# Kernel tuning notes

Measured on AMD Instinct MI355X. Metric: run time of the kernel, lower is better.

The kernel has to match this reference:

```python
import jax, jax.numpy as jnp
import numpy as np
from jax import lax

KS = 10      # kernel_size (asserted == 10 in the torch module)
DCT_N = 10   # dct_n


def _dct_pair(N):
    k = np.arange(N)[:, None]
    i = np.arange(N)[None, :]
    w = np.full((N, 1), np.sqrt(2.0 / N))
    w[0, 0] = np.sqrt(1.0 / N)
    d = w * np.cos(np.pi * (i + 0.5) * k / N)
    return jnp.asarray(d, jnp.float32), jnp.asarray(np.linalg.inv(d), jnp.float32)


def _conv1d(x, w):
    # x: [B, C, L], w: [O, C, K], VALID conv (bias=False in torch)
    return lax.conv_general_dilated(x, w, (1,), 'VALID',
                                    dimension_numbers=('NCH', 'OIH', 'NCH'))


def _two_conv(x, w1, w2):
    return jax.nn.relu(_conv1d(jax.nn.relu(_conv1d(x, w1)), w2))


def _gconv(x, w, att, b):
    # GraphConvolution: att @ (x @ w) + b ; x: [B, node, f_in]
    return jnp.einsum('nm,bmo->bno', att, jnp.einsum('bmf,fo->bmo', x, w)) + b


def _gcn(x, gc1_w, gc1_att, gc1_b, gcb_w, gcb_att, gcb_b, gc7_w, gc7_att, gc7_b):
    # Standard motion-prediction GCN (eval mode: BN=identity, dropout off)
    y = jnp.tanh(_gconv(x, gc1_w, gc1_att, gc1_b))
    for s in range(gcb_w.shape[0]):  # small fixed num_stage
        h = jnp.tanh(_gconv(y, gcb_w[s, 0], gcb_att[s, 0], gcb_b[s, 0]))
        h = jnp.tanh(_gconv(h, gcb_w[s, 1], gcb_att[s, 1], gcb_b[s, 1]))
        y = y + h
    return _gconv(y, gc7_w, gc7_att, gc7_b) + x


def _ffc(x, wl, wg):
    # RealFFC(dim=3): spectral branch (rFFT over time, 1x1 conv on real/imag,
    # ReLU, irFFT) + local 1x1 branch. x: [B, 3, F/3, T]
    y = jnp.fft.rfft(x, axis=-1)
    yc = jnp.concatenate([y.real, y.imag], axis=1)            # [B, 6, F/3, K]
    yc = jax.nn.relu(jnp.einsum('oc,bcfk->bofk', wg, yc))
    re, im = jnp.split(yc, 2, axis=1)
    spec = jnp.fft.irfft(re + 1j * im, n=x.shape[-1], axis=-1)
    return jnp.einsum('oc,bcft->boft', wl, x) + spec


def _forward(input_seq, wq1, wq2, wk1, wk2,
             gc1_w, gc1_att, gc1_b, gcb_w, gcb_att, gcb_b,
             gc7_w, gc7_att, gc7_b, mlp_w1, mlp_w2, ffc_wl, ffc_wg,
             output_n, input_n):
    seq = input_seq[:, :input_n]
    B, _, F = seq.shape
    blen = KS + output_n                       # DCT block length (30)
    dctm, idctm = _dct_pair(blen)
    key_seq = jnp.swapaxes(seq, 1, 2)[:, :, :input_n - output_n]
    query_seq = jnp.swapaxes(seq, 1, 2)[:, :, -KS:]
    # im2col-style overlapping temporal blocks -> per-block DCT
    nvb = input_n - blen + 1
    idx = np.arange(blen)[None, :] + np.arange(nvb)[:, None]
    blocks = seq[:, idx]                       # [B, nvb, blen, F]
    # matches torch reshape(...,dct_n,-1).transpose(2,3).reshape: feature-major
    dvb = jnp.einsum('dk,bnkf->bnfd', dctm[:DCT_N], blocks).reshape(B, nvb, -1)
    key_feat = _two_conv(key_seq / 1000.0, wk1, wk2)       # [B, D, nvb]
    query_feat = _two_conv(query_seq / 1000.0, wq1, wq2)   # [B, D, 1]
    score = jnp.einsum('bdq,bdk->bqk', query_feat, key_feat) + 1e-15
    attn = score / jnp.sum(score, axis=2, keepdims=True)   # sum-normalized attention
    attended = jnp.einsum('bqk,bkf->bqf', attn, dvb)[:, 0].reshape(B, F, DCT_N)
    # FFC branch: pad with last frame x10, fold F into (3, F//3)
    ffc_in = jnp.concatenate([seq, jnp.repeat(seq[:, -1:], 10, axis=1)], axis=1)
    ffc_in = jnp.swapaxes(ffc_in, 1, 2).reshape(B, 3, F // 3, input_n + 10)
    ffc_out = _ffc(ffc_in, ffc_wl, ffc_wg).reshape(B, F, input_n + 10)[:, :, :DCT_N]
    ffc_out = jnp.swapaxes(ffc_out, 1, 2)      # [B, DCT_N, F]
    # GCN branch: last KS frames + last frame repeated output_n times
    gidx = np.concatenate([np.arange(input_n - KS, input_n),
                           np.full(output_n, input_n - 1)])
    gcn_in = seq[:, gidx]                      # [B, blen, F]
    dct_in = jnp.einsum('dk,bkf->bfd', dctm[:DCT_N], gcn_in)
    gcn_out = _gcn(dct_in, gc1_w, gc1_att, gc1_b, gcb_w, gcb_att, gcb_b,
                   gc7_w, gc7_att, gc7_b)      # [B, F, DCT_N]
    combined = jnp.concatenate([gcn_out, attended], axis=-1)
    recon = jnp.einsum('kd,bfd->bkf', idctm[:, :DCT_N], combined[:, :, :DCT_N])  # [B, blen, F]
    fused = jnp.swapaxes(jnp.concatenate([recon, ffc_out], axis=1), 1, 2)  # [B, F, blen+DCT_N=40]
    h = jax.nn.relu(jnp.einsum('bft,ot->bfo', fused, mlp_w1))  # Linear(40,256), no bias
    out = jnp.einsum('bfo,to->bft', h, mlp_w2)                 # Linear(256,40), no bias
    out = jnp.swapaxes(out, 1, 2)[:, :DCT_N]   # [B, DCT_N, F]
    return out[:, :, None, :]                  # [B, DCT_N, itera=1, F]


def setup_inputs() -> dict:
    key = jax.random.key(0)
    ks = jax.random.split(key, 20)
    B, T, F, D, NS = 1024, 50, 48, 512, 2
    p = lambda k, shp: jax.random.normal(k, shp, dtype=jnp.float32) * 0.05
    return {
        'input_seq': jax.random.normal(ks[0], (B, T, F), dtype=jnp.float32),
        'wq1': p(ks[1], (D, F, 6)), 'wq2': p(ks[2], (D, D, 5)),
        'wk1': p(ks[3], (D, F, 6)), 'wk2': p(ks[4], (D, D, 5)),
        'gc1_w': p(ks[5], (10, D)), 'gc1_att': p(ks[6], (F, F)), 'gc1_b': p(ks[7], (D,)),
        'gcb_w': p(ks[8], (NS, 2, D, D)), 'gcb_att': p(ks[9], (NS, 2, F, F)),
        'gcb_b': p(ks[10], (NS, 2, D)),
        'gc7_w': p(ks[11], (D, 10)), 'gc7_att': p(ks[12], (F, F)), 'gc7_b': p(ks[13], (10,)),
        'mlp_w1': p(ks[14], (256, 40)), 'mlp_w2': p(ks[15], (40, 256)),
        'ffc_wl': p(ks[16], (3, 3)), 'ffc_wg': p(ks[17], (6, 6)),
        'output_n': 20, 'input_n': 50, 'itera': 1,
    }


def reference(input_seq, wq1, wq2, wk1, wk2, gc1_w, gc1_att, gc1_b,
              gcb_w, gcb_att, gcb_b, gc7_w, gc7_att, gc7_b,
              mlp_w1, mlp_w2, ffc_wl, ffc_wg, output_n, input_n, itera):
    assert itera == 1  # single-iteration path (the torch itera>1 branch is skipped)
    return _forward(input_seq, wq1, wq2, wk1, wk2,
                    gc1_w, gc1_att, gc1_b, gcb_w, gcb_att, gcb_b,
                    gc7_w, gc7_att, gc7_b, mlp_w1, mlp_w2, ffc_wl, ffc_wg,
                    output_n, input_n)
```

## Files before the change

### kernel.cpp

```cpp
#include <hip/hip_runtime.h>
#include <math.h>

#define BB 1024
#define TT 50
#define FF 48
#define EXTN 60
#define NFREQ 31

typedef _Float16 h8 __attribute__((ext_vector_type(8)));
typedef _Float16 h4 __attribute__((ext_vector_type(4)));
typedef float f4 __attribute__((ext_vector_type(4)));

__device__ __forceinline__ float fast_tanh(float x) {
    float e = __expf(2.0f * x);
    return 1.0f - 2.0f * __builtin_amdgcn_rcpf(e + 1.0f);
}

__global__ void prep_kernel(const float* __restrict__ gcb_w, _Float16* __restrict__ P,
                            const float* __restrict__ gc1_w, _Float16* __restrict__ P1,
                            const float* __restrict__ gc7_w, _Float16* __restrict__ P7,
                            const float* __restrict__ mlp_w1, _Float16* __restrict__ Pw1,
                            const float* __restrict__ mlp_w2, _Float16* __restrict__ Pw2,
                            const float* __restrict__ gc1_att, const float* __restrict__ gcb_att,
                            const float* __restrict__ gc7_att, _Float16* __restrict__ attp,
                            _Float16* __restrict__ Pc_hi, _Float16* __restrict__ Pc_lo,
                            _Float16* __restrict__ Pi_hi, _Float16* __restrict__ Pi_lo,
                            float* __restrict__ dctm, float* __restrict__ dtail) {
    int blk = blockIdx.x, tid = threadIdx.x;
    const _Float16 HZ = (_Float16)0.0f;
    if (blk < 512) {
        int z = blk >> 7;
        int idx = ((blk & 127) << 8) | tid;
        int lane = idx & 63, t8 = idx >> 6;
        int nt = t8 & 7, kw = t8 >> 3;
        int ks = kw & 15, wv = kw >> 4;
        int n = wv * 128 + nt * 16 + (lane & 15);
        int k0 = ks * 32 + (lane >> 4) * 8;
        const float* src = gcb_w + (size_t)z * 262144 + n;
        h8 v;
        #pragma unroll
        for (int j = 0; j < 8; ++j) v[j] = (_Float16)src[(size_t)(k0 + j) * 512];
        *(h8*)(P + (size_t)z * 262144 + (size_t)idx * 8) = v;
    } else if (blk < 528) {
        int idx = ((blk - 512) << 8) | tid;
        int lane = idx & 63, t8 = idx >> 6;
        int nt = t8 & 7, kw = t8 >> 3;
        int ks = kw & 1, wv = kw >> 1;
        int n = wv * 128 + nt * 16 + (lane & 15);
        int k0 = ks * 32 + (lane >> 4) * 8;
        h8 v;
        #pragma unroll
        for (int j = 0; j < 8; ++j) v[j] = (k0 + j < 10) ? (_Float16)gc1_w[(k0 + j) * 512 + n] : HZ;
        *(h8*)(P1 + (size_t)idx * 8) = v;
    } else if (blk < 532) {
        int idx = ((blk - 528) << 8) | tid;
        int lane = idx & 63, t8 = idx >> 6;
        int ks = t8 & 3, wv = t8 >> 2;
        int n = lane & 15;
        int k0 = wv * 128 + ks * 32 + (lane >> 4) * 8;
        h8 v;
        #pragma unroll
        for (int j = 0; j < 8; ++j) v[j] = (n < 10) ? (_Float16)gc7_w[(k0 + j) * 10 + n] : HZ;
        *(h8*)(P7 + (size_t)idx * 8) = v;
    } else if (blk < 540) {
        int idx = ((blk - 532) << 8) | tid;
        int lane = idx & 63, t8 = idx >> 6;
        int ks = t8 & 1, q = t8 >> 1;
        int nt = q & 3, wv = q >> 2;
        int o = wv * 64 + nt * 16 + (lane & 15);
        int k0 = ks * 32 + (lane >> 4) * 8;
        h8 v;
        #pragma unroll
        for (int j = 0; j < 8; ++j) v[j] = (k0 + j < 40) ? (_Float16)mlp_w1[o * 40 + k0 + j] : HZ;
        *(h8*)(Pw1 + (size_t)idx * 8) = v;
    } else if (blk < 542) {
        int idx = ((blk - 540) << 8) | tid;
        int lane = idx & 63, ks = idx >> 6;
        int m = lane & 15;
        int k0 = ks * 32 + (lane >> 4) * 8;
        h8 v;
        #pragma unroll
        for (int j = 0; j < 8; ++j) v[j] = (m < 10) ? (_Float16)mlp_w2[m * 256 + k0 + j] : HZ;
        *(h8*)(Pw2 + (size_t)idx * 8) = v;
    } else if (blk < 614) {
        int idx = (blk - 542) * 256 + tid;
        if (idx < 18432) {
            int l = idx / 3072, r = (idx % 3072) / 64, m = idx & 63;
            float v = 0.f;
            if (m < 48) {
                v = (l == 0) ? gc1_att[r * 48 + m]
                  : (l <= 4) ? gcb_att[(l - 1) * 2304 + r * 48 + m]
                             : gc7_att[r * 48 + m];
            }
            attp[idx] = (_Float16)v;
        }
    } else if (blk < 646) {
        int g = (blk - 614) * 256 + tid;
        int tab = g >> 12, e = g & 4095;
        int j = e & 7, lane = (e >> 3) & 63, t8 = e >> 9;
        int ks = t8 & 1, nt = t8 >> 1;
        int n = nt * 16 + (lane & 15);
        int t = ks * 32 + (lane >> 4) * 8 + j;
        double v = 0.0;
        if (t < 60 && n < 62)
            v = (n < 31) ? cos(M_PI * (double)(n * t) / 30.0)
                         : -sin(M_PI * (double)((n - 31) * t) / 30.0);
        _Float16 hi = (_Float16)(float)v;
        if (tab == 0) Pc_hi[e] = hi;
        else          Pc_lo[e] = (_Float16)(float)(v - (double)(float)hi);
    } else if (blk < 654) {
        int g = (blk - 646) * 256 + tid;
        int tab = g >> 10, e = g & 1023;
        int j = e & 7, lane = (e >> 3) & 63, ks = e >> 9;
        int t = lane & 15;
        int kp = ks * 32 + (lane >> 4) * 8 + j;
        double v = 0.0;
        if (kp == 0) v = 1.0 / 60.0;
        else if (kp < 30) v = (2.0 / 60.0) * cos(M_PI * (double)(kp * t) / 30.0);
        else if (kp == 30) v = ((t & 1) ? -1.0 : 1.0) / 60.0;
        else if (kp >= 32 && kp < 61) v = -(2.0 / 60.0) * sin(M_PI * (double)((kp - 31) * t) / 30.0);
        _Float16 hi = (_Float16)(float)v;
        if (tab == 0) Pi_hi[e] = hi;
        else          Pi_lo[e] = (_Float16)(float)(v - (double)(float)hi);
    } else {
        int idx = (blk - 654) * 256 + tid;
        if (idx < 900) {
            int d = idx / 30, k = idx % 30;
            double w = (d == 0) ? sqrt(1.0 / 30.0) : sqrt(2.0 / 30.0);
            dctm[idx] = (float)(w * cos(M_PI * (k + 0.5) * d / 30.0));
        } else if (idx < 910) {
            int d = idx - 900;
            double w = (d == 0) ? sqrt(1.0 / 30.0) : sqrt(2.0 / 30.0);
            double s = 0.0;
            for (int k = 10; k < 30; ++k) s += w * cos(M_PI * (k + 0.5) * d / 30.0);
            dtail[d] = (float)s;
        }
    }
}

#define S_STRIDE 49152
#define RB_OFF   98304
#define G_OFF    (98304 + 26624)
#define DF_OFF   135168

template<int KSTEPS, int MODE>
__device__ __forceinline__ void gcn_layer(char* smem, char* T,
        const _Float16* __restrict__ Pw, const _Float16* __restrict__ attp,
        const float* __restrict__ bias, h4* sv,
        int lane, int wv8, int l16, int quad) {
    f4 acc[6][4];
    #pragma unroll
    for (int m = 0; m < 6; ++m)
        #pragma unroll
        for (int n = 0; n < 4; ++n) acc[m][n] = (f4)0.0f;

    const _Float16* Pb = Pw + (size_t)(wv8 >> 1) * (KSTEPS * 8 * 512)
                            + (size_t)(wv8 & 1) * 2048 + lane * 8;
    const int xm = l16 & 7;
    __syncthreads();

    #pragma unroll 2
    for (int ks = 0; ks < KSTEPS; ++ks) {
        h8 a[6], bfr[4];
        #pragma unroll
        for (int nt = 0; nt < 4; ++nt)
            bfr[nt] = *(const h8*)(Pb + (ks * 8 + nt) * 512);
        #pragma unroll
        for (int zz = 0; zz < 2; ++zz)
            #pragma unroll
            for (int mt = 0; mt < 3; ++mt)
                a[zz * 3 + mt] = *(h8*)(smem + zz * S_STRIDE + (mt * 16 + l16) * 1024
                                        + (((ks * 4 + quad) ^ xm) << 4));
        #pragma unroll
        for (int m = 0; m < 6; ++m)
            #pragma unroll
            for (int nt = 0; nt < 4; ++nt)
                acc[m][nt] = __builtin_amdgcn_mfma_f32_16x16x32_f16(a[m], bfr[nt], acc[m][nt], 0, 0, 0);
    }

    h8 ab[3][2];
    #pragma unroll
    for (int it = 0; it < 3; ++it)
        #pragma unroll
        for (int ks = 0; ks < 2; ++ks)
            ab[it][ks] = *(const h8*)(attp + (it * 16 + l16) * 64 + ks * 32 + quad * 8);

    __syncthreads();

    #pragma unroll
    for (int mt = 0; mt < 3; ++mt) {
        h4 hv;
        #pragma unroll
        for (int j = 0; j < 4; ++j) hv[j] = (_Float16)acc[mt][0][j];
        *(h4*)(T + l16 * 144 + (mt * 16 + quad * 4) * 2) = hv;
    }
    asm volatile("s_waitcnt lgkmcnt(0)" ::: "memory");
    h8 tf0 = *(h8*)(T + l16 * 144 + quad * 16);
    h8 tf1 = *(h8*)(T + l16 * 144 + 64 + quad * 16);

    #pragma unroll
    for (int e = 0; e < 8; ++e) {
        char* Tn = T + ((e + 1) & 1) * 2304;
        if (e < 7) {
            int zn = (e + 1) >> 2, nn = (e + 1) & 3;
            #pragma unroll
            for (int mt = 0; mt < 3; ++mt) {
                h4 hv;
                #pragma unroll
                for (int j = 0; j < 4; ++j) hv[j] = (_Float16)acc[zn * 3 + mt][nn][j];
                *(h4*)(Tn + l16 * 144 + (mt * 16 + quad * 4) * 2) = hv;
            }
        }
        f4 acc2[3];
        #pragma unroll
        for (int it = 0; it < 3; ++it) {
            acc2[it] = __builtin_amdgcn_mfma_f32_16x16x32_f16(tf0, ab[it][0], (f4)0.0f, 0, 0, 0);
            acc2[it] = __builtin_amdgcn_mfma_f32_16x16x32_f16(tf1, ab[it][1], acc2[it], 0, 0, 0);
        }
        if (e < 7) {
            asm volatile("s_waitcnt lgkmcnt(0)" ::: "memory");
            tf0 = *(h8*)(Tn + l16 * 144 + quad * 16);
            tf1 = *(h8*)(Tn + l16 * 144 + 64 + quad * 16);
        }
        const int z = e >> 2, nt = e & 3;
        const int c0 = wv8 * 64 + nt * 16 + quad * 4;
        const f4 bv = *(const f4*)(bias + c0);
        #pragma unroll
        for (int it = 0; it < 3; ++it) {
            int f = it * 16 + l16;
            char* sp = smem + z * S_STRIDE + f * 1024 + (((c0 >> 3) ^ (f & 7)) << 4) + ((c0 & 7) << 1);
            if (MODE == 1) sv[e * 3 + it] = *(h4*)sp;
            h4 o;
            #pragma unroll
            for (int j = 0; j < 4; ++j) {
                float v = fast_tanh(acc2[it][j] + bv[j]);
                if (MODE == 2) v += (float)sv[e * 3 + it][j];
                o[j] = (_Float16)v;
            }
            *(h4*)sp = o;
        }
    }
}

__launch_bounds__(512, 1)
__global__ void gcn_fused_kernel(const float* __restrict__ seq,
                                 const _Float16* __restrict__ P1,
                                 const _Float16* __restrict__ Pm,
                                 const _Float16* __restrict__ P7,
                                 const _Float16* __restrict__ attp,
                                 const float* __restrict__ gc1_b,
                                 const float* __restrict__ gcb_b,
                                 const float* __restrict__ gc7_b,
                                 const float* __restrict__ dctm,
                                 const float* __restrict__ dtail,
                                 _Float16* __restrict__ fush) {
    __shared__ __align__(16) char smem[139776];
    const int tid = threadIdx.x, lane = tid & 63, wv8 = tid >> 6;
    const int l16 = lane & 15, quad = lane >> 4;
    const int z = tid >> 8, ltid = tid & 255;
    const int b0 = blockIdx.x * 2;
    char* T = smem + RB_OFF + wv8 * 4608;

    {
        char* Rz = smem + RB_OFF + z * 4096;
        char* dctfz = smem + DF_OFF + z * 2304;
        const float* seqb = seq + (size_t)(b0 + z) * 2400;
        if (ltid < 120) *(f4*)(Rz + ltid * 16) = *(const f4*)(seqb + 1920 + ltid * 4);
        for (int v = ltid; v < 310; v += 256)
            ((float*)(Rz + 2048))[v] = (v < 300) ? dctm[v] : dtail[v - 300];
        __syncthreads();
        for (int v = ltid; v < 480; v += 256) {
            int f = v / 10, d = v % 10;
            const float* q = (const float*)Rz;
            const float* L = (const float*)(Rz + 2048);
            float a = L[300 + d] * q[9 * 48 + f];
            #pragma unroll
            for (int k = 0; k < 10; ++k) a += L[d * 30 + k] * q[k * 48 + f];
            ((float*)dctfz)[f * 12 + d] = a;
        }
        __syncthreads();
        for (int v = ltid; v < 384; v += 256) {
            int m = v >> 3, g = v & 7;
            h8 w = (h8)(_Float16)0.0f;
            if (g < 2) {
                #pragma unroll
                for (int j = 0; j < 8; ++j) {
                    int d = g * 8 + j;
                    if (d < 10) w[j] = (_Float16)((float*)dctfz)[m * 12 + d];
                }
            }
            *(h8*)(smem + z * S_STRIDE + m * 1024 + ((g ^ (m & 7)) << 4)) = w;
        }
        for (int v = tid; v < 768; v += 512) {
            int s = v % 3, rr = v / 3;
            int r = rr & 15, wb = rr >> 4;
            *(h8*)(smem + RB_OFF + wb * 2304 + r * 144 + 96 + s * 16) = (h8)(_Float16)0.0f;
        }
    }

    h4 sv[24];
    gcn_layer<2, 0>(smem, T, P1,          attp,          gc1_b,        sv, lane, wv8, l16, quad);
    gcn_layer<16, 1>(smem, T, Pm,          attp + 3072,  gcb_b,        sv, lane, wv8, l16, quad);
    gcn_layer<16, 2>(smem, T, Pm + 262144, attp + 6144,  gcb_b + 512,  sv, lane, wv8, l16, quad);
    gcn_layer<16, 1>(smem, T, Pm + 524288, attp + 9216,  gcb_b + 1024, sv, lane, wv8, l16, quad);
    gcn_layer<16, 2>(smem, T, Pm + 786432, attp + 12288, gcb_b + 1536, sv, lane, wv8, l16, quad);

    __syncthreads();
    {
        const int z6 = wv8 >> 2, wvl = wv8 & 3;
        char* Sz = smem + z6 * S_STRIDE;
        f4 acc[3];
        #pragma unroll
        for (int mt = 0; mt < 3; ++mt) acc[mt] = (f4)0.0f;
        const _Float16* Pb7 = P7 + wvl * 2048 + lane * 8;
        #pragma unroll
        for (int ks = 0; ks < 4; ++ks) {
            h8 bfr = *(const h8*)(Pb7 + ks * 512);
            int kh = wvl * 128 + ks * 32;
            #pragma unroll
            for (int mt = 0; mt < 3; ++mt) {
                h8 a = *(h8*)(Sz + (mt * 16 + l16) * 1024 + ((((kh >> 3) + quad) ^ (l16 & 7)) << 4));
                acc[mt] = __builtin_amdgcn_mfma_f32_16x16x32_f16(a, bfr, acc[mt], 0, 0, 0);
            }
        }
        #pragma unroll
        for (int mt = 0; mt < 3; ++mt)
            *(f4*)(smem + RB_OFF + z6 * 12288 + wvl * 3072 + l16 * 192 + (mt * 16 + quad * 4) * 4) = acc[mt];
    }
    __syncthreads();
    if ((wv8 & 3) == 0) {
        const int z6 = wv8 >> 2;
        char* PZ = smem + RB_OFF + z6 * 12288;
        char* dctfz = smem + DF_OFF + z6 * 2304;
        h4 tw[3]; int ns[3], ms[3];
        #pragma unroll
        for (int q = 0; q < 3; ++q) {
            int idx = lane * 3 + q;
            int n = idx / 12, m0 = (idx % 12) * 4;
            f4 s = *(f4*)(PZ + n * 192 + m0 * 4);
            s += *(f4*)(PZ + 3072 + n * 192 + m0 * 4);
            s += *(f4*)(PZ + 6144 + n * 192 + m0 * 4);
            s += *(f4*)(PZ + 9216 + n * 192 + m0 * 4);
            h4 h;
            #pragma unroll
            for (int j = 0; j < 4; ++j) h[j] = (_Float16)s[j];
            tw[q] = h; ns[q] = n; ms[q] = m0;
        }
        asm volatile("s_waitcnt lgkmcnt(0)" ::: "memory");
        #pragma unroll
        for (int q = 0; q < 3; ++q) *(h4*)(PZ + ns[q] * 144 + ms[q] * 2) = tw[q];
        if (lane < 48) {
            int row = lane / 3, s2 = lane % 3;
            *(h8*)(PZ + row * 144 + 96 + s2 * 16) = (h8)(_Float16)0.0f;
        }
        asm volatile("s_waitcnt lgkmcnt(0)" ::: "memory");
        h8 tf0 = *(h8*)(PZ + l16 * 144 + quad * 16);
        h8 tf1 = *(h8*)(PZ + l16 * 144 + 64 + quad * 16);
        const _Float16* a7 = attp + 15360;
        f4 acc2[3];
        #pragma unroll
        for (int it = 0; it < 3; ++it) {
            h8 ab0 = *(const h8*)(a7 + (it * 16 + l16) * 64 + quad * 8);
            h8 ab1 = *(const h8*)(a7 + (it * 16 + l16) * 64 + 32 + quad * 8);
            acc2[it] = __builtin_amdgcn_mfma_f32_16x16x32_f16(tf0, ab0, (f4)0.0f, 0, 0, 0);
            acc2[it] = __builtin_amdgcn_mfma_f32_16x16x32_f16(tf1, ab1, acc2[it], 0, 0, 0);
        }
        char* G = smem + G_OFF + z6 * 3072;
        #pragma unroll
        for (int it = 0; it < 3; ++it) {
            int f = it * 16 + l16;
            #pragma unroll
            for (int j = 0; j < 4; ++j) {
                int c = quad * 4 + j;
                if (c < 10) {
                    float v = acc2[it][j] + gc7_b[c] + ((float*)dctfz)[f * 12 + c];
                    *(float*)(G + f * 64 + c * 4) = v;
                }
            }
        }
    }
    __syncthreads();
    {
        char* G = smem + G_OFF + z * 3072;
        _Float16* fb = fush + (size_t)(b0 + z) * 3456;
        for (int v = ltid; v < 1440; v += 256) {
            int f = v / 30, t = v % 30;
            float s = 0.f;
            #pragma unroll
            for (int d = 0; d < 10; ++d) s += dctm[d * 30 + t] * *(float*)(G + f * 64 + d * 4);
            fb[f * 72 + t] = (_Float16)s;
        }
        for (int v = ltid; v < 1152; v += 256) {
            int f = v / 24, t = 40 + v % 24;
            fb[f * 72 + t] = (_Float16)0.0f;
        }
    }
}

__launch_bounds__(256, 3)
__global__ void ffc_mlp_kernel(const float* __restrict__ seq,
                               const _Float16* __restrict__ fush,
                               const float* __restrict__ wl,
                               const float* __restrict__ wg,
                               const _Float16* __restrict__ Pw1,
                               const _Float16* __restrict__ Pw2,
                               const _Float16* __restrict__ Pc_hi,
                               const _Float16* __restrict__ Pc_lo,
                               const _Float16* __restrict__ Pi_hi,
                               const _Float16* __restrict__ Pi_lo,
                               float* __restrict__ out) {
    __shared__ __align__(16) char smem[44736];
    float* ext     = (float*)smem;
    char*  extT_hi = smem + 11520;
    char*  extT_lo = smem + 18432;
    char*  Ya_hi   = extT_hi;
    char*  Ya_lo   = extT_lo;
    float* Xre     = (float*)(smem + 25344);
    float* Xim     = (float*)(smem + 31488);
    _Float16* fus  = (_Float16*)(smem + 37632);
    float* wls     = (float*)(smem + 44544);
    float* wgs     = (float*)(smem + 44580);
    _Float16* hlds = (_Float16*)smem;
    char*  R2      = smem + 25344;

    const int b = blockIdx.x, tid = threadIdx.x;
    const int lane = tid & 63, wv = tid >> 6;
    const int l16 = lane & 15, quad = lane >> 4;
    const float* s = seq + (size_t)b * TT * FF;

    for (int idx = tid; idx < EXTN * FF; idx += 256) {
        int t = idx / FF, f = idx % FF;
        ext[idx] = s[(t < TT ? t : TT - 1) * FF + f];
    }
    for (int idx = tid; idx < 64 * FF; idx += 256) {
        int t = idx / FF, f = idx % FF;
        float v = (t < EXTN) ? s[(t < TT ? t : TT - 1) * FF + f] : 0.f;
        _Float16 hi = (_Float16)v;
        ((_Float16*)(extT_hi + f * 144))[t] = hi;
        ((_Float16*)(extT_lo + f * 144))[t] = (_Float16)(v - (float)hi);
    }
    if (tid < 9) wls[tid] = wl[tid];
    if (tid >= 64 && tid < 100) wgs[tid - 64] = wg[tid - 64];
    __syncthreads();

    {
        const int nt = wv;
        f4 acc[3];
        #pragma unroll
        for (int mt = 0; mt < 3; ++mt) acc[mt] = (f4)0.0f;
        #pragma unroll
        for (int ks = 0; ks < 2; ++ks) {
            h8 bhi = *(const h8*)(Pc_hi + (nt * 2 + ks) * 512 + lane * 8);
            h8 blo = *(const h8*)(Pc_lo + (nt * 2 + ks) * 512 + lane * 8);
            #pragma unroll
            for (int mt = 0; mt < 3; ++mt) {
                h8 ahi = *(h8*)(extT_hi + (mt * 16 + l16) * 144 + ks * 64 + quad * 16);
                h8 alo = *(h8*)(extT_lo + (mt * 16 + l16) * 144 + ks * 64 + quad * 16);
                acc[mt] = __builtin_amdgcn_mfma_f32_16x16x32_f16(ahi, bhi, acc[mt], 0, 0, 0);
                acc[mt] = __builtin_amdgcn_mfma_f32_16x16x32_f16(alo, bhi, acc[mt], 0, 0, 0);
                acc[mt] = __builtin_amdgcn_mfma_f32_16x16x32_f16(ahi, blo, acc[mt], 0, 0, 0);
            }
        }
        int n = nt * 16 + l16;
        #pragma unroll
        for (int mt = 0; mt < 3; ++mt)
            #pragma unroll
            for (int i = 0; i < 4; ++i) {
                int f = mt * 16 + quad * 4 + i;
                if (n < 31) Xre[f * 32 + n] = acc[mt][i];
                else if (n < 62) Xim[f * 32 + n - 31] = acc[mt][i];
            }
    }
    for (int v = tid; v < 384; v += 256) {
        int f = v >> 3, g = v & 7;
        *(h8*)((char*)fus + f * 144 + g * 16) =
            *(const h8*)(fush + (size_t)b * 3456 + f * 72 + g * 8);
    }
    __syncthreads();

    for (int idx = tid; idx < 2976; idx += 256) {
        int k = idx % 31; int g = (idx / 31) % 16; int o = idx / (31 * 16);
        float v = wgs[o * 6 + 0] * Xre[g * 32 + k]        + wgs[o * 6 + 1] * Xre[(16 + g) * 32 + k]
                + wgs[o * 6 + 2] * Xre[(32 + g) * 32 + k] + wgs[o * 6 + 3] * Xim[g * 32 + k]
                + wgs[o * 6 + 4] * Xim[(16 + g) * 32 + k] + wgs[o * 6 + 5] * Xim[(32 + g) * 32 + k];
        v = fmaxf(v, 0.f);
        int fr = (o < 3) ? o * 16 + g : (o - 3) * 16 + g;
        int kp = (o < 3) ? k : 31 + k;
        _Float16 hi = (_Float16)v;
        ((_Float16*)(Ya_hi + fr * 144))[kp] = hi;
        ((_Float16*)(Ya_lo + fr * 144))[kp] = (_Float16)(v - (float)hi);
    }
    if (tid < 96) {
        int f = tid >> 1, c = 62 + (tid & 1);
        ((_Float16*)(Ya_hi + f * 144))[c] = (_Float16)0.0f;
        ((_Float16*)(Ya_lo + f * 144))[c] = (_Float16)0.0f;
    }
    __syncthreads();

    if (wv < 3) {
        const int mt = wv;
        f4 ac = (f4)0.0f;
        #pragma unroll
        for (int ks = 0; ks < 2; ++ks) {
            h8 bhi = *(const h8*)(Pi_hi + ks * 512 + lane * 8);
            h8 blo = *(const h8*)(Pi_lo + ks * 512 + lane * 8);
            h8 ahi = *(h8*)(Ya_hi + (mt * 16 + l16) * 144 + ks * 64 + quad * 16);
            h8 alo = *(h8*)(Ya_lo + (mt * 16 + l16) * 144 + ks * 64 + quad * 16);
            ac = __builtin_amdgcn_mfma_f32_16x16x32_f16(ahi, bhi, ac, 0, 0, 0);
            ac = __builtin_amdgcn_mfma_f32_16x16x32_f16(alo, bhi, ac, 0, 0, 0);
            ac = __builtin_amdgcn_mfma_f32_16x16x32_f16(ahi, blo, ac, 0, 0, 0);
        }
        int t = l16;
        if (t < 10) {
            #pragma unroll
            for (int i = 0; i < 4; ++i) {
                int g = quad * 4 + i;
                int f = mt * 16 + g;
                float loc = wls[mt * 3 + 0] * ext[t * FF + g]
                          + wls[mt * 3 + 1] * ext[t * FF + 16 + g]
                          + wls[mt * 3 + 2] * ext[t * FF + 32 + g];
                fus[f * 72 + 30 + t] = (_Float16)(ac[i] + loc);
            }
        }
    }
    __syncthreads();

    f4 acc1[3][4];
    #pragma unroll
    for (int mt = 0; mt < 3; ++mt)
        #pragma unroll
        for (int nt = 0; nt < 4; ++nt) acc1[mt][nt] = (f4)0.0f;
    #pragma unroll
    for (int ks = 0; ks < 2; ++ks) {
        h8 af[3], bf[4];
        #pragma unroll
        for (int mt = 0; mt < 3; ++mt)
            af[mt] = *(h8*)((char*)fus + (mt * 16 + l16) * 144 + ks * 64 + quad * 16);
        #pragma unroll
        for (int nt = 0; nt < 4; ++nt)
            bf[nt] = *(const h8*)(Pw1 + (size_t)(((wv * 4 + nt) * 2 + ks) * 512) + lane * 8);
        #pragma unroll
        for (int mt = 0; mt < 3; ++mt)
            #pragma unroll
            for (int nt = 0; nt < 4; ++nt)
                acc1[mt][nt] = __builtin_amdgcn_mfma_f32_16x16x32_f16(af[mt], bf[nt], acc1[mt][nt], 0, 0, 0);
    }
    __syncthreads();
    #pragma unroll
    for (int mt = 0; mt < 3; ++mt)
        #pragma unroll
        for (int nt = 0; nt < 4; ++nt) {
            int o = wv * 64 + nt * 16 + l16;
            #pragma unroll
            for (int j = 0; j < 4; ++j) {
                int f = mt * 16 + quad * 4 + j;
                hlds[f * 264 + o] = (_Float16)fmaxf(acc1[mt][nt][j], 0.f);
            }
        }
    __syncthreads();
    f4 acc2[3];
    #pragma unroll
    for (int nt3 = 0; nt3 < 3; ++nt3) acc2[nt3] = (f4)0.0f;
    #pragma unroll
    for (int ss = 0; ss < 2; ++ss) {
        int ks = wv * 2 + ss;
        h8 aw = *(const h8*)(Pw2 + (size_t)ks * 512 + lane * 8);
        #pragma unroll
        for (int nt3 = 0; nt3 < 3; ++nt3) {
            h8 bh = *(h8*)((char*)hlds + (nt3 * 16 + l16) * 528 + ks * 64 + quad * 16);
            acc2[nt3] = __builtin_amdgcn_mfma_f32_16x16x32_f16(aw, bh, acc2[nt3], 0, 0, 0);
        }
    }
    #pragma unroll
    for (int nt3 = 0; nt3 < 3; ++nt3)
        *(f4*)(R2 + wv * 3072 + (nt3 * 16 + l16) * 64 + quad * 16) = acc2[nt3];
    __syncthreads();
    for (int v = tid; v < 768; v += 256) {
        int f = v >> 4, t = v & 15;
        float sm = 0.f;
        #pragma unroll
        for (int w4 = 0; w4 < 4; ++w4) sm += *(float*)(R2 + w4 * 3072 + f * 64 + t * 4);
        if (t < 10) out[(size_t)b * 480 + t * 48 + f] = sm;
    }
}

extern "C" void kernel_launch(void* const* d_in, const int* in_sizes, int n_in,
                              void* d_out, int out_size, void* d_ws, size_t ws_size,
                              hipStream_t stream) {
    (void)in_sizes; (void)n_in; (void)out_size;
    const float* seq     = (const float*)d_in[0];
    const float* gc1_w   = (const float*)d_in[5];
    const float* gc1_att = (const float*)d_in[6];
    const float* gc1_b   = (const float*)d_in[7];
    const float* gcb_w   = (const float*)d_in[8];
    const float* gcb_att = (const float*)d_in[9];
    const float* gcb_b   = (const float*)d_in[10];
    const float* gc7_w   = (const float*)d_in[11];
    const float* gc7_att = (const float*)d_in[12];
    const float* gc7_b   = (const float*)d_in[13];
    const float* mlp_w1  = (const float*)d_in[14];
    const float* mlp_w2  = (const float*)d_in[15];
    const float* ffc_wl  = (const float*)d_in[16];
    const float* ffc_wg  = (const float*)d_in[17];
    float* out = (float*)d_out;
    char* ws = (char*)d_ws;

    float*    dctm  = (float*)ws;
    float*    dtail = dctm + 900;
    char*     p0    = ws + 4096;
    _Float16* Pm    = (_Float16*)p0;   p0 += 4 * 262144 * 2;
    _Float16* P1    = (_Float16*)p0;   p0 += 32768 * 2;
    _Float16* P7    = (_Float16*)p0;   p0 += 8192 * 2;
    _Float16* Pw1   = (_Float16*)p0;   p0 += 16384 * 2;
    _Float16* Pw2   = (_Float16*)p0;   p0 += 4096 * 2;
    _Float16* attp  = (_Float16*)p0;   p0 += 18432 * 2;
    _Float16* Pc_hi = (_Float16*)p0;   p0 += 4096 * 2;
    _Float16* Pc_lo = (_Float16*)p0;   p0 += 4096 * 2;
    _Float16* Pi_hi = (_Float16*)p0;   p0 += 1024 * 2;
    _Float16* Pi_lo = (_Float16*)p0;   p0 += 1024 * 2;
    const size_t fixed_bytes = (size_t)(p0 - ws);

    const size_t per_batch = 6912;
    size_t avail = (ws_size > fixed_bytes) ? (ws_size - fixed_bytes) : 0;
    int nc = 1;
    while ((size_t)(BB / nc) * per_batch > avail && nc < 64) nc *= 2;
    int Bc = BB / nc;
    _Float16* fush = (_Float16*)(ws + fixed_bytes);

    prep_kernel<<<658, 256, 0, stream>>>(gcb_w, Pm, gc1_w, P1, gc7_w, P7,
                                         mlp_w1, Pw1, mlp_w2, Pw2,
                                         gc1_att, gcb_att, gc7_att, attp,
                                         Pc_hi, Pc_lo, Pi_hi, Pi_lo, dctm, dtail);

    for (int ci = 0; ci < nc; ++ci) {
        const float* seqc = seq + (size_t)ci * Bc * TT * FF;
        float* outc = out + (size_t)ci * Bc * 480;
        gcn_fused_kernel<<<Bc / 2, 512, 0, stream>>>(seqc, P1, Pm, P7, attp,
                                                     gc1_b, gcb_b, gc7_b, dctm, dtail, fush);
        ffc_mlp_kernel<<<Bc, 256, 0, stream>>>(seqc, fush, ffc_wl, ffc_wg, Pw1, Pw2,
                                               Pc_hi, Pc_lo, Pi_hi, Pi_lo, outc);
    }
}
```

Baseline: 267.2 us.

## Fuse FFC/MLP stage into GCN kernel, keep intermediate in shared memory

```diff
diff --git a/kernel.cpp b/kernel.cpp
--- a/kernel.cpp
+++ b/kernel.cpp
@@ -253,7 +253,15 @@
                                  const float* __restrict__ gc7_b,
                                  const float* __restrict__ dctm,
                                  const float* __restrict__ dtail,
-                                 _Float16* __restrict__ fush) {
+                                 const float* __restrict__ wl,
+                                 const float* __restrict__ wg,
+                                 const _Float16* __restrict__ Pw1,
+                                 const _Float16* __restrict__ Pw2,
+                                 const _Float16* __restrict__ Pc_hi,
+                                 const _Float16* __restrict__ Pc_lo,
+                                 const _Float16* __restrict__ Pi_hi,
+                                 const _Float16* __restrict__ Pi_lo,
+                                 float* __restrict__ out) {
     __shared__ __align__(16) char smem[139776];
     const int tid = threadIdx.x, lane = tid & 63, wv8 = tid >> 6;
     const int l16 = lane & 15, quad = lane >> 4;
@@ -382,7 +390,7 @@
     __syncthreads();
     {
         char* G = smem + G_OFF + z * 3072;
-        _Float16* fb = fush + (size_t)(b0 + z) * 3456;
+        _Float16* fb = (_Float16*)(smem + z * 44736 + 37632);
         for (int v = ltid; v < 1440; v += 256) {
             int f = v / 30, t = v % 30;
             float s = 0.f;
@@ -395,199 +403,180 @@
             fb[f * 72 + t] = (_Float16)0.0f;
         }
     }
-}
-
-__launch_bounds__(256, 3)
-__global__ void ffc_mlp_kernel(const float* __restrict__ seq,
-                               const _Float16* __restrict__ fush,
-                               const float* __restrict__ wl,
-                               const float* __restrict__ wg,
-                               const _Float16* __restrict__ Pw1,
-                               const _Float16* __restrict__ Pw2,
-                               const _Float16* __restrict__ Pc_hi,
-                               const _Float16* __restrict__ Pc_lo,
-                               const _Float16* __restrict__ Pi_hi,
-                               const _Float16* __restrict__ Pi_lo,
-                               float* __restrict__ out) {
-    __shared__ __align__(16) char smem[44736];
-    float* ext     = (float*)smem;
-    char*  extT_hi = smem + 11520;
-    char*  extT_lo = smem + 18432;
-    char*  Ya_hi   = extT_hi;
-    char*  Ya_lo   = extT_lo;
-    float* Xre     = (float*)(smem + 25344);
-    float* Xim     = (float*)(smem + 31488);
-    _Float16* fus  = (_Float16*)(smem + 37632);
-    float* wls     = (float*)(smem + 44544);
-    float* wgs     = (float*)(smem + 44580);
-    _Float16* hlds = (_Float16*)smem;
-    char*  R2      = smem + 25344;
-
-    const int b = blockIdx.x, tid = threadIdx.x;
-    const int lane = tid & 63, wv = tid >> 6;
-    const int l16 = lane & 15, quad = lane >> 4;
-    const float* s = seq + (size_t)b * TT * FF;
-
-    for (int idx = tid; idx < EXTN * FF; idx += 256) {
-        int t = idx / FF, f = idx % FF;
-        ext[idx] = s[(t < TT ? t : TT - 1) * FF + f];
-    }
-    for (int idx = tid; idx < 64 * FF; idx += 256) {
-        int t = idx / FF, f = idx % FF;
-        float v = (t < EXTN) ? s[(t < TT ? t : TT - 1) * FF + f] : 0.f;
-        _Float16 hi = (_Float16)v;
-        ((_Float16*)(extT_hi + f * 144))[t] = hi;
-        ((_Float16*)(extT_lo + f * 144))[t] = (_Float16)(v - (float)hi);
-    }
-    if (tid < 9) wls[tid] = wl[tid];
-    if (tid >= 64 && tid < 100) wgs[tid - 64] = wg[tid - 64];
-    __syncthreads();
 
     {
-        const int nt = wv;
-        f4 acc[3];
-        #pragma unroll
-        for (int mt = 0; mt < 3; ++mt) acc[mt] = (f4)0.0f;
+        char* FP = smem + z * 44736;
+        float* ext     = (float*)FP;
+        char*  extT_hi = FP + 11520;
+        char*  extT_lo = FP + 18432;
+        char*  Ya_hi   = extT_hi;
+        char*  Ya_lo   = extT_lo;
+        float* Xre     = (float*)(FP + 25344);
+        float* Xim     = (float*)(FP + 31488);
+        _Float16* fus  = (_Float16*)(FP + 37632);
+        float* wls     = (float*)(FP + 44544);
+        float* wgs     = (float*)(FP + 44580);
+        _Float16* hlds = (_Float16*)FP;
+        char*  R2      = FP + 25344;
+        const int fwv = (tid >> 6) & 3;
+        const float* sq = seq + (size_t)(b0 + z) * TT * FF;
+
+        for (int idx = ltid; idx < EXTN * FF; idx += 256) {
+            int t = idx / FF, f = idx % FF;
+            ext[idx] = sq[(t < TT ? t : TT - 1) * FF + f];
+        }
+        for (int idx = ltid; idx < 64 * FF; idx += 256) {
+            int t = idx / FF, f = idx % FF;
+            float v = (t < EXTN) ? sq[(t < TT ? t : TT - 1) * FF + f] : 0.f;
+            _Float16 hi = (_Float16)v;
+            ((_Float16*)(extT_hi + f * 144))[t] = hi;
+            ((_Float16*)(extT_lo + f * 144))[t] = (_Float16)(v - (float)hi);
+        }
+        if (ltid < 9) wls[ltid] = wl[ltid];
+        if (ltid >= 64 && ltid < 100) wgs[ltid - 64] = wg[ltid - 64];
+        __syncthreads();
+
+        {
+            const int nt = fwv;
+            f4 acc[3];
+            #pragma unroll
+            for (int mt = 0; mt < 3; ++mt) acc[mt] = (f4)0.0f;
+            #pragma unroll
+            for (int ks = 0; ks < 2; ++ks) {
+                h8 bhi = *(const h8*)(Pc_hi + (nt * 2 + ks) * 512 + lane * 8);
+                h8 blo = *(const h8*)(Pc_lo + (nt * 2 + ks) * 512 + lane * 8);
+                #pragma unroll
+                for (int mt = 0; mt < 3; ++mt) {
+                    h8 ahi = *(h8*)(extT_hi + (mt * 16 + l16) * 144 + ks * 64 + quad * 16);
+                    h8 alo = *(h8*)(extT_lo + (mt * 16 + l16) * 144 + ks * 64 + quad * 16);
+                    acc[mt] = __builtin_amdgcn_mfma_f32_16x16x32_f16(ahi, bhi, acc[mt], 0, 0, 0);
+                    acc[mt] = __builtin_amdgcn_mfma_f32_16x16x32_f16(alo, bhi, acc[mt], 0, 0, 0);
+                    acc[mt] = __builtin_amdgcn_mfma_f32_16x16x32_f16(ahi, blo, acc[mt], 0, 0, 0);
+                }
+            }
+            int n = nt * 16 + l16;
+            #pragma unroll
+            for (int mt = 0; mt < 3; ++mt)
+                #pragma unroll
+                for (int i = 0; i < 4; ++i) {
+                    int f = mt * 16 + quad * 4 + i;
+                    if (n < 31) Xre[f * 32 + n] = acc[mt][i];
+                    else if (n < 62) Xim[f * 32 + n - 31] = acc[mt][i];
+                }
+        }
+        __syncthreads();
+
+        for (int idx = ltid; idx < 2976; idx += 256) {
+            int k = idx % 31; int g = (idx / 31) % 16; int o = idx / (31 * 16);
+            float v = wgs[o * 6 + 0] * Xre[g * 32 + k]        + wgs[o * 6 + 1] * Xre[(16 + g) * 32 + k]
+                    + wgs[o * 6 + 2] * Xre[(32 + g) * 32 + k] + wgs[o * 6 + 3] * Xim[g * 32 + k]
+                    + wgs[o * 6 + 4] * Xim[(16 + g) * 32 + k] + wgs[o * 6 + 5] * Xim[(32 + g) * 32 + k];
+            v = fmaxf(v, 0.f);
+            int fr = (o < 3) ? o * 16 + g : (o - 3) * 16 + g;
+            int kp = (o < 3) ? k : 31 + k;
+            _Float16 hi = (_Float16)v;
+            ((_Float16*)(Ya_hi + fr * 144))[kp] = hi;
+            ((_Float16*)(Ya_lo + fr * 144))[kp] = (_Float16)(v - (float)hi);
+        }
+        if (ltid < 96) {
+            int f = ltid >> 1, c = 62 + (ltid & 1);
+            ((_Float16*)(Ya_hi + f * 144))[c] = (_Float16)0.0f;
+            ((_Float16*)(Ya_lo + f * 144))[c] = (_Float16)0.0f;
+        }
+        __syncthreads();
+
+        if (fwv < 3) {
+            const int mt = fwv;
+            f4 ac = (f4)0.0f;
+            #pragma unroll
+            for (int ks = 0; ks < 2; ++ks) {
+                h8 bhi = *(const h8*)(Pi_hi + ks * 512 + lane * 8);
+                h8 blo = *(const h8*)(Pi_lo + ks * 512 + lane * 8);
+                h8 ahi = *(h8*)(Ya_hi + (mt * 16 + l16) * 144 + ks * 64 + quad * 16);
+                h8 alo = *(h8*)(Ya_lo + (mt * 16 + l16) * 144 + ks * 64 + quad * 16);
+                ac = __builtin_amdgcn_mfma_f32_16x16x32_f16(ahi, bhi, ac, 0, 0, 0);
+                ac = __builtin_amdgcn_mfma_f32_16x16x32_f16(alo, bhi, ac, 0, 0, 0);
+                ac = __builtin_amdgcn_mfma_f32_16x16x32_f16(ahi, blo, ac, 0, 0, 0);
+            }
+            int t = l16;
+            if (t < 10) {
+                #pragma unroll
+                for (int i = 0; i < 4; ++i) {
+                    int g = quad * 4 + i;
+                    int f = mt * 16 + g;
+                    float loc = wls[mt * 3 + 0] * ext[t * FF + g]
+                              + wls[mt * 3 + 1] * ext[t * FF + 16 + g]
+                              + wls[mt * 3 + 2] * ext[t * FF + 32 + g];
+                    fus[f * 72 + 30 + t] = (_Float16)(ac[i] + loc);
+                }
+            }
+        }
+        __syncthreads();
+
+        f4 acc1[3][4];
+        #pragma unroll
+        for (int mt = 0; mt < 3; ++mt)
+            #pragma unroll
+            for (int nt = 0; nt < 4; ++nt) acc1[mt][nt] = (f4)0.0f;
         #pragma unroll
         for (int ks = 0; ks < 2; ++ks) {
-            h8 bhi = *(const h8*)(Pc_hi + (nt * 2 + ks) * 512 + lane * 8);
-            h8 blo = *(const h8*)(Pc_lo + (nt * 2 + ks) * 512 + lane * 8);
-            #pragma unroll
-            for (int mt = 0; mt < 3; ++mt) {
-                h8 ahi = *(h8*)(extT_hi + (mt * 16 + l16) * 144 + ks * 64 + quad * 16);
-                h8 alo = *(h8*)(extT_lo + (mt * 16 + l16) * 144 + ks * 64 + quad * 16);
-                acc[mt] = __builtin_amdgcn_mfma_f32_16x16x32_f16(ahi, bhi, acc[mt], 0, 0, 0);
-                acc[mt] = __builtin_amdgcn_mfma_f32_16x16x32_f16(alo, bhi, acc[mt], 0, 0, 0);
-                acc[mt] = __builtin_amdgcn_mfma_f32_16x16x32_f16(ahi, blo, acc[mt], 0, 0, 0);
-            }
-        }
-        int n = nt * 16 + l16;
+            h8 af[3], bf[4];
+            #pragma unroll
+            for (int mt = 0; mt < 3; ++mt)
+                af[mt] = *(h8*)((char*)fus + (mt * 16 + l16) * 144 + ks * 64 + quad * 16);
+            #pragma unroll
+            for (int nt = 0; nt < 4; ++nt)
+                bf[nt] = *(const h8*)(Pw1 + (size_t)(((fwv * 4 + nt) * 2 + ks) * 512) + lane * 8);
+            #pragma unroll
+            for (int mt = 0; mt < 3; ++mt)
+                #pragma unroll
+                for (int nt = 0; nt < 4; ++nt)
+                    acc1[mt][nt] = __builtin_amdgcn_mfma_f32_16x16x32_f16(af[mt], bf[nt], acc1[mt][nt], 0, 0, 0);
+        }
+        __syncthreads();
         #pragma unroll
         for (int mt = 0; mt < 3; ++mt)
             #pragma unroll
-            for (int i = 0; i < 4; ++i) {
-                int f = mt * 16 + quad * 4 + i;
-                if (n < 31) Xre[f * 32 + n] = acc[mt][i];
-                else if (n < 62) Xim[f * 32 + n - 31] = acc[mt][i];
-            }
-    }
-    for (int v = tid; v < 384; v += 256) {
-        int f = v >> 3, g = v & 7;
-        *(h8*)((char*)fus + f * 144 + g * 16) =
-            *(const h8*)(fush + (size_t)b * 3456 + f * 72 + g * 8);
-    }
-    __syncthreads();
-
-    for (int idx = tid; idx < 2976; idx += 256) {
-        int k = idx % 31; int g = (idx / 31) % 16; int o = idx / (31 * 16);
-        float v = wgs[o * 6 + 0] * Xre[g * 32 + k]        + wgs[o * 6 + 1] * Xre[(16 + g) * 32 + k]
-                + wgs[o * 6 + 2] * Xre[(32 + g) * 32 + k] + wgs[o * 6 + 3] * Xim[g * 32 + k]
-                + wgs[o * 6 + 4] * Xim[(16 + g) * 32 + k] + wgs[o * 6 + 5] * Xim[(32 + g) * 32 + k];
-        v = fmaxf(v, 0.f);
-        int fr = (o < 3) ? o * 16 + g : (o - 3) * 16 + g;
-        int kp = (o < 3) ? k : 31 + k;
-        _Float16 hi = (_Float16)v;
-        ((_Float16*)(Ya_hi + fr * 144))[kp] = hi;
-        ((_Float16*)(Ya_lo + fr * 144))[kp] = (_Float16)(v - (float)hi);
-    }
-    if (tid < 96) {
-        int f = tid >> 1, c = 62 + (tid & 1);
-        ((_Float16*)(Ya_hi + f * 144))[c] = (_Float16)0.0f;
-        ((_Float16*)(Ya_lo + f * 144))[c] = (_Float16)0.0f;
-    }
-    __syncthreads();
-
-    if (wv < 3) {
-        const int mt = wv;
-        f4 ac = (f4)0.0f;
-        #pragma unroll
-        for (int ks = 0; ks < 2; ++ks) {
-            h8 bhi = *(const h8*)(Pi_hi + ks * 512 + lane * 8);
-            h8 blo = *(const h8*)(Pi_lo + ks * 512 + lane * 8);
-            h8 ahi = *(h8*)(Ya_hi + (mt * 16 + l16) * 144 + ks * 64 + quad * 16);
-            h8 alo = *(h8*)(Ya_lo + (mt * 16 + l16) * 144 + ks * 64 + quad * 16);
-            ac = __builtin_amdgcn_mfma_f32_16x16x32_f16(ahi, bhi, ac, 0, 0, 0);
-            ac = __builtin_amdgcn_mfma_f32_16x16x32_f16(alo, bhi, ac, 0, 0, 0);
-            ac = __builtin_amdgcn_mfma_f32_16x16x32_f16(ahi, blo, ac, 0, 0, 0);
-        }
-        int t = l16;
-        if (t < 10) {
-            #pragma unroll
-            for (int i = 0; i < 4; ++i) {
-                int g = quad * 4 + i;
-                int f = mt * 16 + g;
-                float loc = wls[mt * 3 + 0] * ext[t * FF + g]
-                          + wls[mt * 3 + 1] * ext[t * FF + 16 + g]
-                          + wls[mt * 3 + 2] * ext[t * FF + 32 + g];
-                fus[f * 72 + 30 + t] = (_Float16)(ac[i] + loc);
-            }
-        }
-    }
-    __syncthreads();
-
-    f4 acc1[3][4];
-    #pragma unroll
-    for (int mt = 0; mt < 3; ++mt)
-        #pragma unroll
-        for (int nt = 0; nt < 4; ++nt) acc1[mt][nt] = (f4)0.0f;
-    #pragma unroll
-    for (int ks = 0; ks < 2; ++ks) {
-        h8 af[3], bf[4];
-        #pragma unroll
-        for (int mt = 0; mt < 3; ++mt)
-            af[mt] = *(h8*)((char*)fus + (mt * 16 + l16) * 144 + ks * 64 + quad * 16);
-        #pragma unroll
-        for (int nt = 0; nt < 4; ++nt)
-            bf[nt] = *(const h8*)(Pw1 + (size_t)(((wv * 4 + nt) * 2 + ks) * 512) + lane * 8);
-        #pragma unroll
-        for (int mt = 0; mt < 3; ++mt)
-            #pragma unroll
-            for (int nt = 0; nt < 4; ++nt)
-                acc1[mt][nt] = __builtin_amdgcn_mfma_f32_16x16x32_f16(af[mt], bf[nt], acc1[mt][nt], 0, 0, 0);
-    }
-    __syncthreads();
-    #pragma unroll
-    for (int mt = 0; mt < 3; ++mt)
-        #pragma unroll
-        for (int nt = 0; nt < 4; ++nt) {
-            int o = wv * 64 + nt * 16 + l16;
-            #pragma unroll
-            for (int j = 0; j < 4; ++j) {
-                int f = mt * 16 + quad * 4 + j;
-                hlds[f * 264 + o] = (_Float16)fmaxf(acc1[mt][nt][j], 0.f);
-            }
-        }
-    __syncthreads();
-    f4 acc2[3];
-    #pragma unroll
-    for (int nt3 = 0; nt3 < 3; ++nt3) acc2[nt3] = (f4)0.0f;
-    #pragma unroll
-    for (int ss = 0; ss < 2; ++ss) {
-        int ks = wv * 2 + ss;
-        h8 aw = *(const h8*)(Pw2 + (size_t)ks * 512 + lane * 8);
-        #pragma unroll
-        for (int nt3 = 0; nt3 < 3; ++nt3) {
-            h8 bh = *(h8*)((char*)hlds + (nt3 * 16 + l16) * 528 + ks * 64 + quad * 16);
-            acc2[nt3] = __builtin_amdgcn_mfma_f32_16x16x32_f16(aw, bh, acc2[nt3], 0, 0, 0);
-        }
-    }
-    #pragma unroll
-    for (int nt3 = 0; nt3 < 3; ++nt3)
-        *(f4*)(R2 + wv * 3072 + (nt3 * 16 + l16) * 64 + quad * 16) = acc2[nt3];
-    __syncthreads();
-    for (int v = tid; v < 768; v += 256) {
-        int f = v >> 4, t = v & 15;
-        float sm = 0.f;
-        #pragma unroll
-        for (int w4 = 0; w4 < 4; ++w4) sm += *(float*)(R2 + w4 * 3072 + f * 64 + t * 4);
-        if (t < 10) out[(size_t)b * 480 + t * 48 + f] = sm;
+            for (int nt = 0; nt < 4; ++nt) {
+                int o = fwv * 64 + nt * 16 + l16;
+                #pragma unroll
+                for (int j = 0; j < 4; ++j) {
+                    int f = mt * 16 + quad * 4 + j;
+                    hlds[f * 264 + o] = (_Float16)fmaxf(acc1[mt][nt][j], 0.f);
+                }
+            }
+        __syncthreads();
+        f4 acc2[3];
+        #pragma unroll
+        for (int nt3 = 0; nt3 < 3; ++nt3) acc2[nt3] = (f4)0.0f;
+        #pragma unroll
+        for (int ss = 0; ss < 2; ++ss) {
+            int ks = fwv * 2 + ss;
+            h8 aw = *(const h8*)(Pw2 + (size_t)ks * 512 + lane * 8);
+            #pragma unroll
+            for (int nt3 = 0; nt3 < 3; ++nt3) {
+                h8 bh = *(h8*)((char*)hlds + (nt3 * 16 + l16) * 528 + ks * 64 + quad * 16);
+                acc2[nt3] = __builtin_amdgcn_mfma_f32_16x16x32_f16(aw, bh, acc2[nt3], 0, 0, 0);
+            }
+        }
+        #pragma unroll
+        for (int nt3 = 0; nt3 < 3; ++nt3)
+            *(f4*)(R2 + fwv * 3072 + (nt3 * 16 + l16) * 64 + quad * 16) = acc2[nt3];
+        __syncthreads();
+        for (int v = ltid; v < 768; v += 256) {
+            int f = v >> 4, t = v & 15;
+            float sm = 0.f;
+            #pragma unroll
+            for (int w4 = 0; w4 < 4; ++w4) sm += *(float*)(R2 + w4 * 3072 + f * 64 + t * 4);
+            if (t < 10) out[(size_t)(b0 + z) * 480 + t * 48 + f] = sm;
+        }
     }
 }
 
 extern "C" void kernel_launch(void* const* d_in, const int* in_sizes, int n_in,
                               void* d_out, int out_size, void* d_ws, size_t ws_size,
                               hipStream_t stream) {
-    (void)in_sizes; (void)n_in; (void)out_size;
+    (void)in_sizes; (void)n_in; (void)out_size; (void)ws_size;
     const float* seq     = (const float*)d_in[0];
     const float* gc1_w   = (const float*)d_in[5];
     const float* gc1_att = (const float*)d_in[6];
@@ -618,26 +607,14 @@
     _Float16* Pc_lo = (_Float16*)p0;   p0 += 4096 * 2;
     _Float16* Pi_hi = (_Float16*)p0;   p0 += 1024 * 2;
     _Float16* Pi_lo = (_Float16*)p0;   p0 += 1024 * 2;
-    const size_t fixed_bytes = (size_t)(p0 - ws);
-
-    const size_t per_batch = 6912;
-    size_t avail = (ws_size > fixed_bytes) ? (ws_size - fixed_bytes) : 0;
-    int nc = 1;
-    while ((size_t)(BB / nc) * per_batch > avail && nc < 64) nc *= 2;
-    int Bc = BB / nc;
-    _Float16* fush = (_Float16*)(ws + fixed_bytes);
 
     prep_kernel<<<658, 256, 0, stream>>>(gcb_w, Pm, gc1_w, P1, gc7_w, P7,
                                          mlp_w1, Pw1, mlp_w2, Pw2,
                                          gc1_att, gcb_att, gc7_att, attp,
                                          Pc_hi, Pc_lo, Pi_hi, Pi_lo, dctm, dtail);
 
-    for (int ci = 0; ci < nc; ++ci) {
-        const float* seqc = seq + (size_t)ci * Bc * TT * FF;
-        float* outc = out + (size_t)ci * Bc * 480;
-        gcn_fused_kernel<<<Bc / 2, 512, 0, stream>>>(seqc, P1, Pm, P7, attp,
-                                                     gc1_b, gcb_b, gc7_b, dctm, dtail, fush);
-        ffc_mlp_kernel<<<Bc, 256, 0, stream>>>(seqc, fush, ffc_wl, ffc_wg, Pw1, Pw2,
-                                               Pc_hi, Pc_lo, Pi_hi, Pi_lo, outc);
-    }
+    gcn_fused_kernel<<<BB / 2, 512, 0, stream>>>(seq, P1, Pm, P7, attp,
+                                                 gc1_b, gcb_b, gc7_b, dctm, dtail,
+                                                 ffc_wl, ffc_wg, Pw1, Pw2,
+                                                 Pc_hi, Pc_lo, Pi_hi, Pi_lo, out);
 }
```

After: 269.6 us. Within noise of the previous version (+0.9%).
